# Kernel tuning notes

Measured on AMD Instinct MI355X. Metric: run time of the kernel, lower is better.

## Reference

```python
import jax, jax.numpy as jnp
import numpy as np

B, L, V, D = 8, 128, 32000, 64
R1, R2, UP = 2 * D, 5 * D, 10 * D  # first_reduce, second_reduce, up_scale defaults


def pos_enc(seq_len, d, n=10000.0):
    # matches getPositionEncoding: P[k,2i]=sin(k/n^(2i/d)), P[k,2i+1]=cos(k/n^(2i/d))
    k = jnp.arange(seq_len, dtype=jnp.float32)[:, None]
    i = jnp.arange(d // 2, dtype=jnp.float32)[None, :]
    ang = k / (n ** (2.0 * i / d))
    return jnp.stack([jnp.sin(ang), jnp.cos(ang)], axis=-1).reshape(seq_len, d)


def setup_inputs() -> dict:
    key = jax.random.key(0)
    ks = jax.random.split(key, 20)

    def lin(k, out_f, in_f):
        bound = 1.0 / np.sqrt(in_f)
        k1, k2 = jax.random.split(k)
        W = jax.random.uniform(k1, (out_f, in_f), jnp.float32, -bound, bound)
        b = jax.random.uniform(k2, (out_f,), jnp.float32, -bound, bound)
        return W, b

    inp = {"x": jax.random.uniform(ks[0], (B, L, V), jnp.float32)}
    inp["W_emb"], inp["b_emb"] = lin(ks[1], D, V)
    inp["W_pos1"], inp["b_pos1"] = lin(ks[2], D, 2 * D)
    inp["W_red"], inp["b_red"] = lin(ks[3], R1, L * D)
    inp["W_pos2"], inp["b_pos2"] = lin(ks[4], R1, 2 * R1)
    inp["W_red2"], inp["b_red2"] = lin(ks[5], R2, L * R1)
    inp["W_pos3"], inp["b_pos3"] = lin(ks[6], R2, 2 * R2)
    inp["W_up1"], inp["b_up1"] = lin(ks[7], UP, R2)
    inp["W_up2"], inp["b_up2"] = lin(ks[8], V, UP)
    inp["W_fin"], inp["b_fin"] = lin(ks[9], 1, L)
    return inp


def reference(x, W_emb, b_emb, W_pos1, b_pos1, W_red, b_red, W_pos2, b_pos2,
              W_red2, b_red2, W_pos3, b_pos3, W_up1, b_up1, W_up2, b_up2,
              W_fin, b_fin):
    relu = jax.nn.relu
    P1 = pos_enc(L, 2 * D)   # [L, 2D]
    P2 = pos_enc(L, 2 * R1)  # [L, 2*R1]
    P3 = pos_enc(L, 2 * R2)  # [L, 2*R2]

    h = relu(x @ W_emb.T + b_emb)                       # [B, L, D]
    h = h + relu(P1 @ W_pos1.T + b_pos1)[None]          # learned sin pos emb

    # einsum('bij,bkm->bikj'): out[b,i,k,j] = h[b,i,j] * sum_m h[b,k,m]
    s = h.sum(-1)                                       # [B, L]
    h = (h[:, :, None, :] * s[:, None, :, None]).reshape(B, L, L * D)
    h = relu(h @ W_red.T + b_red)                       # [B, L, R1]
    h = h + relu(P2 @ W_pos2.T + b_pos2)[None]

    s = h.sum(-1)                                       # [B, L]
    h = (h[:, :, None, :] * s[:, None, :, None]).reshape(B, L, L * R1)
    h = relu(h @ W_red2.T + b_red2)                     # [B, L, R2]
    h = h + relu(P3 @ W_pos3.T + b_pos3)[None]

    h = relu(h @ W_up1.T + b_up1)                       # [B, L, UP]
    h = relu(h @ W_up2.T + b_up2)                       # [B, L, V]
    # transpose(1,2) then Linear(L->1), relu, squeeze
    out = relu(jnp.einsum('blv,l->bv', h, W_fin[0]) + b_fin[0])  # [B, V]
    return out
```

## Files before the change

kernel.cpp:

```cpp
#include <hip/hip_runtime.h>
#include <hip/hip_bf16.h>
#include <math.h>

#define B_  8
#define L_  128
#define V_  32000
#define D_  64
#define R1_ 128
#define R2_ 320
#define UP_ 640
#define SPLITS_ 50

typedef short bf16x8 __attribute__((ext_vector_type(8)));
typedef float f32x4 __attribute__((ext_vector_type(4)));

#define GLDS16(gp, lp)                                                         \
    __builtin_amdgcn_global_load_lds(                                          \
        (const __attribute__((address_space(1))) void*)(gp),                   \
        (__attribute__((address_space(3))) void*)(lp), 16, 0, 0)

static __device__ inline unsigned short f2bf(float x) {
    __hip_bfloat16 h = __float2bfloat16(x);
    return *reinterpret_cast<unsigned short*>(&h);
}

static __device__ inline void split1(float v, unsigned short& h, unsigned short& l) {
    unsigned short hb = f2bf(v);
    float hf = __uint_as_float(((unsigned int)hb) << 16);
    h = hb;
    l = f2bf(v - hf);
}
static __device__ inline void split4(float4 v, ushort4& h, ushort4& l) {
    split1(v.x, h.x, l.x);
    split1(v.y, h.y, l.y);
    split1(v.z, h.z, l.z);
    split1(v.w, h.w, l.w);
}

__global__ __launch_bounds__(256) void pe_kernel(const float* __restrict__ W,
                                                 const float* __restrict__ bias,
                                                 float* __restrict__ out,
                                                 int outF, int dEnc) {
    __shared__ float P[640];
    int l = blockIdx.x;
    int t = threadIdx.x;
    for (int m = t; m < dEnc; m += 256) {
        int i = m >> 1;
        float ang = (float)l * powf(10000.0f, -2.0f * (float)i / (float)dEnc);
        P[m] = (m & 1) ? cosf(ang) : sinf(ang);
    }
    __syncthreads();
    for (int o = t; o < outF; o += 256) {
        float acc = bias[o];
        const float* w = W + (size_t)o * dEnc;
        for (int m = 0; m < dEnc; ++m) acc = fmaf(P[m], w[m], acc);
        out[l * outF + o] = fmaxf(acc, 0.f);
    }
}

__global__ __launch_bounds__(256) void embA_mfma(const float* __restrict__ x,
                                                 const float* __restrict__ Wemb,
                                                 float* __restrict__ partA) {
    __shared__ short lds[16384];
    const int XH = 0, XL = 4096, WH = 8192, WL = 12288;

    int t = threadIdx.x;
    int lane = t & 63, w = t >> 6;
    int ln = lane & 15, lg = lane >> 4;
    int sr = t >> 2, sc = t & 3;
    int rb = blockIdx.x, ks = blockIdx.y;
    int row0 = rb * 64;
    int mrow = w * 16 + ln;

    f32x4 acc[4];
#pragma unroll
    for (int nt = 0; nt < 4; ++nt) acc[nt] = (f32x4){0.f, 0.f, 0.f, 0.f};

    for (int ch = 0; ch < 640 / 64; ++ch) {
        int k0 = ks * 640 + ch * 64;
        const float* xrow = x + (size_t)(row0 + sr) * 32000 + k0;
        const float* wrow = Wemb + (size_t)sr * 32000 + k0;
        __syncthreads();
#pragma unroll
        for (int i = 0; i < 4; ++i) {
            int k = sc * 4 + 16 * i;
            int idx = ((k >> 3) * 64 + sr) * 8 + (k & 7);
            float4 v = *(const float4*)(xrow + k);
            ushort4 h, l;
            split4(v, h, l);
            *(ushort4*)&lds[XH + idx] = h;
            *(ushort4*)&lds[XL + idx] = l;
            float4 wv = *(const float4*)(wrow + k);
            split4(wv, h, l);
            *(ushort4*)&lds[WH + idx] = h;
            *(ushort4*)&lds[WL + idx] = l;
        }
        __syncthreads();
#pragma unroll
        for (int kstep = 0; kstep < 2; ++kstep) {
            int ga = kstep * 4 + lg;
            bf16x8 ah = *(const bf16x8*)&lds[XH + (ga * 64 + mrow) * 8];
            bf16x8 al = *(const bf16x8*)&lds[XL + (ga * 64 + mrow) * 8];
#pragma unroll
            for (int nt = 0; nt < 4; ++nt) {
                int nrow = nt * 16 + ln;
                bf16x8 bh = *(const bf16x8*)&lds[WH + (ga * 64 + nrow) * 8];
                bf16x8 bl = *(const bf16x8*)&lds[WL + (ga * 64 + nrow) * 8];
                acc[nt] = __builtin_amdgcn_mfma_f32_16x16x32_bf16(ah, bh, acc[nt], 0, 0, 0);
                acc[nt] = __builtin_amdgcn_mfma_f32_16x16x32_bf16(ah, bl, acc[nt], 0, 0, 0);
                acc[nt] = __builtin_amdgcn_mfma_f32_16x16x32_bf16(al, bh, acc[nt], 0, 0, 0);
            }
        }
    }
#pragma unroll
    for (int nt = 0; nt < 4; ++nt)
#pragma unroll
        for (int r = 0; r < 4; ++r)
            partA[((size_t)ks * 1024 + row0 + w * 16 + lg * 4 + r) * 64 + nt * 16 + ln] =
                acc[nt][r];
}

__global__ __launch_bounds__(64) void reduceA_kernel(const float* __restrict__ partA,
                                                     const float* __restrict__ bemb,
                                                     const float* __restrict__ pe1,
                                                     float* __restrict__ h1,
                                                     float* __restrict__ s1) {
    int row = blockIdx.x;
    int d = threadIdx.x;
    int l = row & 127;
    float v = bemb[d];
    for (int s = 0; s < SPLITS_; ++s) v += partA[((size_t)s * 1024 + row) * 64 + d];
    v = fmaxf(v, 0.f) + pe1[l * 64 + d];
    h1[row * 64 + d] = v;
    float sum = v;
    for (int off = 32; off > 0; off >>= 1) sum += __shfl_down(sum, off);
    if (d == 0) s1[row] = sum;
}

__global__ __launch_bounds__(64) void wr1_kernel(const float* __restrict__ Wred,
                                                 const float* __restrict__ s1,
                                                 float* __restrict__ Wr1) {
    __shared__ float ss[8 * 128];
    int r = blockIdx.x;
    int j = threadIdx.x;
    for (int idx = j; idx < 1024; idx += 64) ss[idx] = s1[idx];
    __syncthreads();
    float acc[8];
#pragma unroll
    for (int b = 0; b < 8; ++b) acc[b] = 0.f;
    const float* w = Wred + (size_t)r * 8192 + j;
    for (int k = 0; k < 128; ++k) {
        float wv = w[k * 64];
#pragma unroll
        for (int b = 0; b < 8; ++b) acc[b] = fmaf(ss[b * 128 + k], wv, acc[b]);
    }
#pragma unroll
    for (int b = 0; b < 8; ++b) Wr1[((size_t)b * 128 + r) * 64 + j] = acc[b];
}

__global__ __launch_bounds__(128) void h2_kernel(const float* __restrict__ h1,
                                                 const float* __restrict__ Wr1,
                                                 const float* __restrict__ bred,
                                                 const float* __restrict__ pe2,
                                                 float* __restrict__ h2,
                                                 float* __restrict__ s2) {
    __shared__ float hrow[64];
    __shared__ float red[2];
    int row = blockIdx.x;
    int b = row >> 7, i = row & 127;
    int r = threadIdx.x;
    if (r < 64) hrow[r] = h1[row * 64 + r];
    __syncthreads();
    float acc = bred[r];
    const float4* w = (const float4*)(Wr1 + ((size_t)b * 128 + r) * 64);
#pragma unroll
    for (int j4 = 0; j4 < 16; ++j4) {
        float4 wv = w[j4];
        float4 hv = *(const float4*)&hrow[j4 * 4];
        acc = fmaf(hv.x, wv.x, acc);
        acc = fmaf(hv.y, wv.y, acc);
        acc = fmaf(hv.z, wv.z, acc);
        acc = fmaf(hv.w, wv.w, acc);
    }
    float val = fmaxf(acc, 0.f) + pe2[i * 128 + r];
    h2[row * 128 + r] = val;
    float sum = val;
    for (int off = 32; off > 0; off >>= 1) sum += __shfl_down(sum, off);
    if ((r & 63) == 0) red[r >> 6] = sum;
    __syncthreads();
    if (r == 0) s2[row] = red[0] + red[1];
}

__global__ __launch_bounds__(128) void wr2_kernel(const float* __restrict__ Wred2,
                                                  const float* __restrict__ s2,
                                                  float* __restrict__ Wr2) {
    __shared__ float ss[8 * 128];
    int r = blockIdx.x;
    int j = threadIdx.x;
    for (int idx = j; idx < 1024; idx += 128) ss[idx] = s2[idx];
    __syncthreads();
    float acc[8];
#pragma unroll
    for (int b = 0; b < 8; ++b) acc[b] = 0.f;
    const float* w = Wred2 + (size_t)r * 16384 + j;
    for (int k = 0; k < 128; ++k) {
        float wv = w[k * 128];
#pragma unroll
        for (int b = 0; b < 8; ++b) acc[b] = fmaf(ss[b * 128 + k], wv, acc[b]);
    }
#pragma unroll
    for (int b = 0; b < 8; ++b) Wr2[((size_t)b * 320 + r) * 128 + j] = acc[b];
}

__global__ __launch_bounds__(320) void h3_kernel(const float* __restrict__ h2,
                                                 const float* __restrict__ Wr2,
                                                 const float* __restrict__ bred2,
                                                 const float* __restrict__ pe3,
                                                 float* __restrict__ h3) {
    __shared__ float hrow[128];
    int row = blockIdx.x;
    int b = row >> 7, i = row & 127;
    int r = threadIdx.x;
    if (r < 128) hrow[r] = h2[row * 128 + r];
    __syncthreads();
    float acc = bred2[r];
    const float4* w = (const float4*)(Wr2 + ((size_t)b * 320 + r) * 128);
#pragma unroll
    for (int j4 = 0; j4 < 32; ++j4) {
        float4 wv = w[j4];
        float4 hv = *(const float4*)&hrow[j4 * 4];
        acc = fmaf(hv.x, wv.x, acc);
        acc = fmaf(hv.y, wv.y, acc);
        acc = fmaf(hv.z, wv.z, acc);
        acc = fmaf(hv.w, wv.w, acc);
    }
    h3[(size_t)row * 320 + r] = fmaxf(acc, 0.f) + pe3[i * 320 + r];
}

__global__ __launch_bounds__(320) void h4_kernel(const float* __restrict__ h3,
                                                 const float* __restrict__ Wup1,
                                                 const float* __restrict__ bup1,
                                                 unsigned short* __restrict__ h4b) {
    __shared__ float hs[8 * 320];
    int rowbase = blockIdx.x * 8;
    int t = threadIdx.x;
    for (int idx = t; idx < 8 * 320; idx += 320) hs[idx] = h3[(size_t)rowbase * 320 + idx];
    __syncthreads();
    for (int uu = 0; uu < 2; ++uu) {
        int u = t + uu * 320;
        float bias = bup1[u];
        float acc[8];
#pragma unroll
        for (int q = 0; q < 8; ++q) acc[q] = bias;
        const float4* w = (const float4*)(Wup1 + (size_t)u * 320);
        for (int j4 = 0; j4 < 80; ++j4) {
            float4 wv = w[j4];
#pragma unroll
            for (int q = 0; q < 8; ++q) {
                float4 hv = *(const float4*)&hs[q * 320 + j4 * 4];
                acc[q] = fmaf(hv.x, wv.x, acc[q]);
                acc[q] = fmaf(hv.y, wv.y, acc[q]);
                acc[q] = fmaf(hv.z, wv.z, acc[q]);
                acc[q] = fmaf(hv.w, wv.w, acc[q]);
            }
        }
#pragma unroll
        for (int q = 0; q < 8; ++q)
            h4b[((size_t)rowbase + q) * 640 + u] = f2bf(fmaxf(acc[q], 0.f));
    }
}

__global__ __launch_bounds__(256) void conv_bf16(const float* __restrict__ src,
                                                 unsigned short* __restrict__ dst,
                                                 int n4) {
    int stride = gridDim.x * 256;
    for (int i = blockIdx.x * 256 + threadIdx.x; i < n4; i += stride) {
        float4 v = ((const float4*)src)[i];
        ushort4 o;
        o.x = f2bf(v.x); o.y = f2bf(v.y); o.z = f2bf(v.z); o.w = f2bf(v.w);
        ((ushort4*)dst)[i] = o;
    }
}

__global__ __launch_bounds__(256) void final_mfma_kernel(
    const unsigned short* __restrict__ h4b,
    const unsigned short* __restrict__ Wup2b,
    const float* __restrict__ bup2,
    const float* __restrict__ Wfin,
    const float* __restrict__ bfin,
    float* __restrict__ out) {
    __shared__ short tile[16384];
    __shared__ float redbuf[256];

    int t = threadIdx.x;
    int lane = t & 63;
    int w = t >> 6;
    int wv = w >> 1, wl = w & 1;
    int ln = lane & 15, lg = lane >> 4;
    int b = blockIdx.y;
    int v0 = blockIdx.x * 128;

    const char* Ag = (const char*)Wup2b;
    const char* Bg = (const char*)h4b;
    bool isA = (w < 2);
    int seg = (isA ? w : (w - 2)) * 8192;

    f32x4 acc[4][4];
#pragma unroll
    for (int mt = 0; mt < 4; ++mt)
#pragma unroll
        for (int nt = 0; nt < 4; ++nt) acc[mt][nt] = (f32x4){0.f, 0.f, 0.f, 0.f};

    for (int ch = 0; ch < 10; ++ch) {
        int k0 = ch * 64;
        __syncthreads();
#pragma unroll
        for (int s = 0; s < 8; ++s) {
            int F = seg + s * 1024 + lane * 16;
            int r = F >> 7;
            int g = ((F >> 4) & 7) ^ (r & 7);
            size_t rowG = isA ? (size_t)(v0 + r) : (size_t)(b * 128 + r);
            const char* gp = (isA ? Ag : Bg) + (rowG * 640 + (size_t)(k0 + g * 8)) * 2;
            char* lp = (char*)tile + (isA ? 0 : 16384) + seg + s * 1024;
            GLDS16(gp, lp);
        }
        __syncthreads();
#pragma unroll
        for (int ks = 0; ks < 2; ++ks) {
            bf16x8 aF[4], bF[4];
#pragma unroll
            for (int mt = 0; mt < 4; ++mt) {
                int rA = wv * 64 + mt * 16 + ln;
                int g = ks * 4 + lg;
                int off = rA * 128 + ((g ^ (rA & 7)) * 16);
                aF[mt] = *(const bf16x8*)((const char*)tile + off);
            }
#pragma unroll
            for (int nt = 0; nt < 4; ++nt) {
                int rB = wl * 64 + nt * 16 + ln;
                int g = ks * 4 + lg;
                int off = 16384 + rB * 128 + ((g ^ (rB & 7)) * 16);
                bF[nt] = *(const bf16x8*)((const char*)tile + off);
            }
#pragma unroll
            for (int mt = 0; mt < 4; ++mt)
#pragma unroll
                for (int nt = 0; nt < 4; ++nt)
                    acc[mt][nt] = __builtin_amdgcn_mfma_f32_16x16x32_bf16(
                        aF[mt], bF[nt], acc[mt][nt], 0, 0, 0);
        }
    }

    float bfin0 = bfin[0];
#pragma unroll
    for (int mt = 0; mt < 4; ++mt) {
        float bu[4];
#pragma unroll
        for (int r = 0; r < 4; ++r)
            bu[r] = bup2[v0 + wv * 64 + mt * 16 + lg * 4 + r];
        float part[4] = {0.f, 0.f, 0.f, 0.f};
#pragma unroll
        for (int nt = 0; nt < 4; ++nt) {
            float wf = Wfin[wl * 64 + nt * 16 + ln];
#pragma unroll
            for (int r = 0; r < 4; ++r)
                part[r] += wf * fmaxf(acc[mt][nt][r] + bu[r], 0.f);
        }
#pragma unroll
        for (int off = 8; off >= 1; off >>= 1)
#pragma unroll
            for (int r = 0; r < 4; ++r) part[r] += __shfl_xor(part[r], off, 64);
        if (ln == 0) {
#pragma unroll
            for (int r = 0; r < 4; ++r)
                redbuf[wl * 128 + wv * 64 + mt * 16 + lg * 4 + r] = part[r];
        }
    }
    __syncthreads();
    if (t < 128) {
        float vsum = redbuf[t] + redbuf[128 + t] + bfin0;
        out[(size_t)b * 32000 + v0 + t] = fmaxf(vsum, 0.f);
    }
}

extern "C" void kernel_launch(void* const* d_in, const int* in_sizes, int n_in,
                              void* d_out, int out_size, void* d_ws, size_t ws_size,
                              hipStream_t stream) {
    const float* x      = (const float*)d_in[0];
    const float* W_emb  = (const float*)d_in[1];
    const float* b_emb  = (const float*)d_in[2];
    const float* W_pos1 = (const float*)d_in[3];
    const float* b_pos1 = (const float*)d_in[4];
    const float* W_red  = (const float*)d_in[5];
    const float* b_red  = (const float*)d_in[6];
    const float* W_pos2 = (const float*)d_in[7];
    const float* b_pos2 = (const float*)d_in[8];
    const float* W_red2 = (const float*)d_in[9];
    const float* b_red2 = (const float*)d_in[10];
    const float* W_pos3 = (const float*)d_in[11];
    const float* b_pos3 = (const float*)d_in[12];
    const float* W_up1  = (const float*)d_in[13];
    const float* b_up1  = (const float*)d_in[14];
    const float* W_up2  = (const float*)d_in[15];
    const float* b_up2  = (const float*)d_in[16];
    const float* W_fin  = (const float*)d_in[17];
    const float* b_fin  = (const float*)d_in[18];
    float* out = (float*)d_out;

    float* ws  = (float*)d_ws;
    float* pe1 = ws;
    float* pe2 = pe1 + 8192;
    float* pe3 = pe2 + 16384;
    float* h1  = pe3 + 40960;
    float* s1  = h1 + 65536;
    float* Wr1 = s1 + 1024;
    float* h2  = Wr1 + 65536;
    float* s2  = h2 + 131072;
    float* Wr2 = s2 + 1024;
    float* h3  = Wr2 + 327680;
    unsigned short* h4b   = (unsigned short*)(h3 + 327680);
    unsigned short* Wup2b = (unsigned short*)((float*)h4b + 327680);
    float* partA = (float*)Wup2b;

    pe_kernel<<<dim3(128), 256, 0, stream>>>(W_pos1, b_pos1, pe1, 64, 128);
    pe_kernel<<<dim3(128), 256, 0, stream>>>(W_pos2, b_pos2, pe2, 128, 256);
    pe_kernel<<<dim3(128), 256, 0, stream>>>(W_pos3, b_pos3, pe3, 320, 640);
    embA_mfma<<<dim3(16, SPLITS_), 256, 0, stream>>>(x, W_emb, partA);
    reduceA_kernel<<<dim3(1024), 64, 0, stream>>>(partA, b_emb, pe1, h1, s1);
    conv_bf16<<<dim3(4096), 256, 0, stream>>>(W_up2, Wup2b, (V_ * UP_) / 4);
    wr1_kernel<<<dim3(128), 64, 0, stream>>>(W_red, s1, Wr1);
    h2_kernel<<<dim3(1024), 128, 0, stream>>>(h1, Wr1, b_red, pe2, h2, s2);
    wr2_kernel<<<dim3(320), 128, 0, stream>>>(W_red2, s2, Wr2);
    h3_kernel<<<dim3(1024), 320, 0, stream>>>(h2, Wr2, b_red2, pe3, h3);
    h4_kernel<<<dim3(128), 320, 0, stream>>>(h3, W_up1, b_up1, h4b);
    final_mfma_kernel<<<dim3(250, 8), 256, 0, stream>>>(h4b, Wup2b, b_up2, W_fin,
                                                        b_fin, out);
}
```

Before: 534.3 us.

## Pre-split W_emb to bf16, double-buffer embedding GEMM, transpose weights for coalescing

Pre-converts W_emb into hi/lo bf16 arrays in a separate kernel. The embedding GEMM then streams them into LDS with global_load_lds double buffering, while x is loaded into registers and split per lane. Split-K goes from 50 to 100 slices. W_pos and W_up1 are transposed so the pe and h4 kernels read coalesced columns, and h4 is regridded. This adds several extra preprocessing kernels and workspace each call, and doubles the partial-sum traffic in reduceA.

```diff
diff --git a/kernel.cpp b/kernel.cpp
--- a/kernel.cpp
+++ b/kernel.cpp
@@ -9,7 +9,7 @@
 #define R1_ 128
 #define R2_ 320
 #define UP_ 640
-#define SPLITS_ 50
+#define SPLITS_ 100
 
 typedef short bf16x8 __attribute__((ext_vector_type(8)));
 typedef float f32x4 __attribute__((ext_vector_type(4)));
@@ -30,87 +30,136 @@
     h = hb;
     l = f2bf(v - hf);
 }
-static __device__ inline void split4(float4 v, ushort4& h, ushort4& l) {
-    split1(v.x, h.x, l.x);
-    split1(v.y, h.y, l.y);
-    split1(v.z, h.z, l.z);
-    split1(v.w, h.w, l.w);
-}
-
-__global__ __launch_bounds__(256) void pe_kernel(const float* __restrict__ W,
+
+__global__ __launch_bounds__(256) void transpose_f32(const float* __restrict__ src,
+                                                     float* __restrict__ dst,
+                                                     int R, int C) {
+    int idx = blockIdx.x * 256 + threadIdx.x;
+    if (idx < R * C) {
+        int c = idx / R, r = idx - c * R;
+        dst[idx] = src[(size_t)r * C + c];
+    }
+}
+
+__global__ __launch_bounds__(256) void convW_emb(const float* __restrict__ Wemb,
+                                                 unsigned short* __restrict__ Whb,
+                                                 unsigned short* __restrict__ Wlb) {
+    int u = blockIdx.x * 256 + threadIdx.x;
+    int kb = u >> 6, row = u & 63;
+    const float* s = Wemb + (size_t)row * 32000 + kb * 8;
+    unsigned short h8[8], l8[8];
+#pragma unroll
+    for (int j = 0; j < 8; ++j) split1(s[j], h8[j], l8[j]);
+    *(ushort4*)&Whb[(size_t)u * 8]     = *(ushort4*)&h8[0];
+    *(ushort4*)&Whb[(size_t)u * 8 + 4] = *(ushort4*)&h8[4];
+    *(ushort4*)&Wlb[(size_t)u * 8]     = *(ushort4*)&l8[0];
+    *(ushort4*)&Wlb[(size_t)u * 8 + 4] = *(ushort4*)&l8[4];
+}
+
+__global__ __launch_bounds__(320) void pe_kernel(const float* __restrict__ WT,
                                                  const float* __restrict__ bias,
                                                  float* __restrict__ out,
                                                  int outF, int dEnc) {
     __shared__ float P[640];
     int l = blockIdx.x;
     int t = threadIdx.x;
-    for (int m = t; m < dEnc; m += 256) {
+    for (int m = t; m < dEnc; m += outF) {
         int i = m >> 1;
         float ang = (float)l * powf(10000.0f, -2.0f * (float)i / (float)dEnc);
         P[m] = (m & 1) ? cosf(ang) : sinf(ang);
     }
     __syncthreads();
-    for (int o = t; o < outF; o += 256) {
-        float acc = bias[o];
-        const float* w = W + (size_t)o * dEnc;
-        for (int m = 0; m < dEnc; ++m) acc = fmaf(P[m], w[m], acc);
-        out[l * outF + o] = fmaxf(acc, 0.f);
-    }
+    float acc = bias[t];
+#pragma unroll 4
+    for (int m = 0; m < dEnc; ++m) acc = fmaf(P[m], WT[(size_t)m * outF + t], acc);
+    out[l * outF + t] = fmaxf(acc, 0.f);
 }
 
 __global__ __launch_bounds__(256) void embA_mfma(const float* __restrict__ x,
-                                                 const float* __restrict__ Wemb,
+                                                 const unsigned short* __restrict__ Whb,
+                                                 const unsigned short* __restrict__ Wlb,
                                                  float* __restrict__ partA) {
     __shared__ short lds[16384];
-    const int XH = 0, XL = 4096, WH = 8192, WL = 12288;
-
     int t = threadIdx.x;
     int lane = t & 63, w = t >> 6;
     int ln = lane & 15, lg = lane >> 4;
-    int sr = t >> 2, sc = t & 3;
     int rb = blockIdx.x, ks = blockIdx.y;
     int row0 = rb * 64;
-    int mrow = w * 16 + ln;
+    const float* xrow = x + (size_t)(row0 + w * 16 + ln) * 32000;
 
     f32x4 acc[4];
 #pragma unroll
     for (int nt = 0; nt < 4; ++nt) acc[nt] = (f32x4){0.f, 0.f, 0.f, 0.f};
 
-    for (int ch = 0; ch < 640 / 64; ++ch) {
-        int k0 = ks * 640 + ch * 64;
-        const float* xrow = x + (size_t)(row0 + sr) * 32000 + k0;
-        const float* wrow = Wemb + (size_t)sr * 32000 + k0;
+    float4 xc[4], xn[4];
+
+    {
+        int kb0 = (ks * 320) >> 3;
+#pragma unroll
+        for (int s = 0; s < 4; ++s) {
+            int ubase = s * 256 + w * 64;
+            const unsigned short* arr = (s < 2) ? Whb : Wlb;
+            int uu = (s < 2) ? ubase : (ubase - 512);
+            const char* gp = (const char*)arr + ((size_t)kb0 * 64 + uu + lane) * 16;
+            char* lp = (char*)lds + ((s < 2) ? 0 : 8192) + uu * 16;
+            GLDS16(gp, lp);
+        }
+        const float* bp = xrow + ks * 320 + lg * 8;
+        xc[0] = ((const float4*)bp)[0];
+        xc[1] = ((const float4*)bp)[1];
+        xc[2] = ((const float4*)(bp + 32))[0];
+        xc[3] = ((const float4*)(bp + 32))[1];
+    }
+
+#pragma unroll
+    for (int ch = 0; ch < 5; ++ch) {
         __syncthreads();
-#pragma unroll
-        for (int i = 0; i < 4; ++i) {
-            int k = sc * 4 + 16 * i;
-            int idx = ((k >> 3) * 64 + sr) * 8 + (k & 7);
-            float4 v = *(const float4*)(xrow + k);
-            ushort4 h, l;
-            split4(v, h, l);
-            *(ushort4*)&lds[XH + idx] = h;
-            *(ushort4*)&lds[XL + idx] = l;
-            float4 wv = *(const float4*)(wrow + k);
-            split4(wv, h, l);
-            *(ushort4*)&lds[WH + idx] = h;
-            *(ushort4*)&lds[WL + idx] = l;
-        }
-        __syncthreads();
+        if (ch < 4) {
+            int kb0 = (ks * 320 + (ch + 1) * 64) >> 3;
+            int p = (ch + 1) & 1;
+#pragma unroll
+            for (int s = 0; s < 4; ++s) {
+                int ubase = s * 256 + w * 64;
+                const unsigned short* arr = (s < 2) ? Whb : Wlb;
+                int uu = (s < 2) ? ubase : (ubase - 512);
+                const char* gp = (const char*)arr + ((size_t)kb0 * 64 + uu + lane) * 16;
+                char* lp = (char*)lds + p * 16384 + ((s < 2) ? 0 : 8192) + uu * 16;
+                GLDS16(gp, lp);
+            }
+            const float* bp = xrow + ks * 320 + (ch + 1) * 64 + lg * 8;
+            xn[0] = ((const float4*)bp)[0];
+            xn[1] = ((const float4*)bp)[1];
+            xn[2] = ((const float4*)(bp + 32))[0];
+            xn[3] = ((const float4*)(bp + 32))[1];
+        }
+        bf16x8 ah[2], al[2];
 #pragma unroll
         for (int kstep = 0; kstep < 2; ++kstep) {
-            int ga = kstep * 4 + lg;
-            bf16x8 ah = *(const bf16x8*)&lds[XH + (ga * 64 + mrow) * 8];
-            bf16x8 al = *(const bf16x8*)&lds[XL + (ga * 64 + mrow) * 8];
+            float f[8] = {xc[2 * kstep].x, xc[2 * kstep].y, xc[2 * kstep].z, xc[2 * kstep].w,
+                          xc[2 * kstep + 1].x, xc[2 * kstep + 1].y, xc[2 * kstep + 1].z,
+                          xc[2 * kstep + 1].w};
+            unsigned short h8[8], l8[8];
+#pragma unroll
+            for (int j = 0; j < 8; ++j) split1(f[j], h8[j], l8[j]);
+            ah[kstep] = *(bf16x8*)h8;
+            al[kstep] = *(bf16x8*)l8;
+        }
+        const char* buf = (const char*)lds + (ch & 1) * 16384;
+#pragma unroll
+        for (int kstep = 0; kstep < 2; ++kstep) {
+            int g = kstep * 4 + lg;
 #pragma unroll
             for (int nt = 0; nt < 4; ++nt) {
                 int nrow = nt * 16 + ln;
-                bf16x8 bh = *(const bf16x8*)&lds[WH + (ga * 64 + nrow) * 8];
-                bf16x8 bl = *(const bf16x8*)&lds[WL + (ga * 64 + nrow) * 8];
-                acc[nt] = __builtin_amdgcn_mfma_f32_16x16x32_bf16(ah, bh, acc[nt], 0, 0, 0);
-                acc[nt] = __builtin_amdgcn_mfma_f32_16x16x32_bf16(ah, bl, acc[nt], 0, 0, 0);
-                acc[nt] = __builtin_amdgcn_mfma_f32_16x16x32_bf16(al, bh, acc[nt], 0, 0, 0);
+                bf16x8 bh = *(const bf16x8*)(buf + (g * 64 + nrow) * 16);
+                bf16x8 bl = *(const bf16x8*)(buf + 8192 + (g * 64 + nrow) * 16);
+                acc[nt] = __builtin_amdgcn_mfma_f32_16x16x32_bf16(ah[kstep], bh, acc[nt], 0, 0, 0);
+                acc[nt] = __builtin_amdgcn_mfma_f32_16x16x32_bf16(ah[kstep], bl, acc[nt], 0, 0, 0);
+                acc[nt] = __builtin_amdgcn_mfma_f32_16x16x32_bf16(al[kstep], bh, acc[nt], 0, 0, 0);
             }
         }
+#pragma unroll
+        for (int i = 0; i < 4; ++i) xc[i] = xn[i];
     }
 #pragma unroll
     for (int nt = 0; nt < 4; ++nt)
@@ -129,6 +178,7 @@
     int d = threadIdx.x;
     int l = row & 127;
     float v = bemb[d];
+#pragma unroll 4
     for (int s = 0; s < SPLITS_; ++s) v += partA[((size_t)s * 1024 + row) * 64 + d];
     v = fmaxf(v, 0.f) + pe1[l * 64 + d];
     h1[row * 64 + d] = v;
@@ -238,36 +288,33 @@
 }
 
 __global__ __launch_bounds__(320) void h4_kernel(const float* __restrict__ h3,
-                                                 const float* __restrict__ Wup1,
+                                                 const float* __restrict__ Wup1T,
                                                  const float* __restrict__ bup1,
                                                  unsigned short* __restrict__ h4b) {
-    __shared__ float hs[8 * 320];
-    int rowbase = blockIdx.x * 8;
+    __shared__ float hsT[320 * 4];
     int t = threadIdx.x;
-    for (int idx = t; idx < 8 * 320; idx += 320) hs[idx] = h3[(size_t)rowbase * 320 + idx];
-    __syncthreads();
-    for (int uu = 0; uu < 2; ++uu) {
-        int u = t + uu * 320;
-        float bias = bup1[u];
-        float acc[8];
-#pragma unroll
-        for (int q = 0; q < 8; ++q) acc[q] = bias;
-        const float4* w = (const float4*)(Wup1 + (size_t)u * 320);
-        for (int j4 = 0; j4 < 80; ++j4) {
-            float4 wv = w[j4];
-#pragma unroll
-            for (int q = 0; q < 8; ++q) {
-                float4 hv = *(const float4*)&hs[q * 320 + j4 * 4];
-                acc[q] = fmaf(hv.x, wv.x, acc[q]);
-                acc[q] = fmaf(hv.y, wv.y, acc[q]);
-                acc[q] = fmaf(hv.z, wv.z, acc[q]);
-                acc[q] = fmaf(hv.w, wv.w, acc[q]);
-            }
-        }
-#pragma unroll
-        for (int q = 0; q < 8; ++q)
-            h4b[((size_t)rowbase + q) * 640 + u] = f2bf(fmaxf(acc[q], 0.f));
-    }
+    int row0 = blockIdx.x * 4;
+    int u = blockIdx.y * 320 + t;
+    for (int idx = t; idx < 1280; idx += 320) {
+        int q = idx / 320, j = idx - q * 320;
+        hsT[j * 4 + q] = h3[(size_t)(row0 + q) * 320 + j];
+    }
+    __syncthreads();
+    float acc[4] = {0.f, 0.f, 0.f, 0.f};
+    const float* wt = Wup1T + u;
+#pragma unroll 4
+    for (int j = 0; j < 320; ++j) {
+        float wv = wt[(size_t)j * 640];
+        float4 hv = *(const float4*)&hsT[j * 4];
+        acc[0] = fmaf(hv.x, wv, acc[0]);
+        acc[1] = fmaf(hv.y, wv, acc[1]);
+        acc[2] = fmaf(hv.z, wv, acc[2]);
+        acc[3] = fmaf(hv.w, wv, acc[3]);
+    }
+    float bias = bup1[u];
+#pragma unroll
+    for (int q = 0; q < 4; ++q)
+        h4b[(size_t)(row0 + q) * 640 + u] = f2bf(fmaxf(acc[q] + bias, 0.f));
 }
 
 __global__ __launch_bounds__(256) void conv_bf16(const float* __restrict__ src,
@@ -420,19 +467,33 @@
     float* h3  = Wr2 + 327680;
     unsigned short* h4b   = (unsigned short*)(h3 + 327680);
     unsigned short* Wup2b = (unsigned short*)((float*)h4b + 327680);
+    float* after = (float*)Wup2b + 10240000;
+    float* WposT1 = after;
+    float* WposT2 = WposT1 + 8192;
+    float* WposT3 = WposT2 + 32768;
+    float* Wup1T  = WposT3 + 204800;
+    unsigned short* Whb = (unsigned short*)(Wup1T + 204800);
+    unsigned short* Wlb = Whb + 2048000;
     float* partA = (float*)Wup2b;
 
-    pe_kernel<<<dim3(128), 256, 0, stream>>>(W_pos1, b_pos1, pe1, 64, 128);
-    pe_kernel<<<dim3(128), 256, 0, stream>>>(W_pos2, b_pos2, pe2, 128, 256);
-    pe_kernel<<<dim3(128), 256, 0, stream>>>(W_pos3, b_pos3, pe3, 320, 640);
-    embA_mfma<<<dim3(16, SPLITS_), 256, 0, stream>>>(x, W_emb, partA);
+    convW_emb<<<dim3(1000), 256, 0, stream>>>(W_emb, Whb, Wlb);
+    transpose_f32<<<dim3(32), 256, 0, stream>>>(W_pos1, WposT1, 64, 128);
+    transpose_f32<<<dim3(128), 256, 0, stream>>>(W_pos2, WposT2, 128, 256);
+    transpose_f32<<<dim3(800), 256, 0, stream>>>(W_pos3, WposT3, 320, 640);
+    transpose_f32<<<dim3(800), 256, 0, stream>>>(W_up1, Wup1T, 640, 320);
+
+    pe_kernel<<<dim3(128), 64, 0, stream>>>(WposT1, b_pos1, pe1, 64, 128);
+    pe_kernel<<<dim3(128), 128, 0, stream>>>(WposT2, b_pos2, pe2, 128, 256);
+    pe_kernel<<<dim3(128), 320, 0, stream>>>(WposT3, b_pos3, pe3, 320, 640);
+
+    embA_mfma<<<dim3(16, SPLITS_), 256, 0, stream>>>(x, Whb, Wlb, partA);
     reduceA_kernel<<<dim3(1024), 64, 0, stream>>>(partA, b_emb, pe1, h1, s1);
     conv_bf16<<<dim3(4096), 256, 0, stream>>>(W_up2, Wup2b, (V_ * UP_) / 4);
     wr1_kernel<<<dim3(128), 64, 0, stream>>>(W_red, s1, Wr1);
     h2_kernel<<<dim3(1024), 128, 0, stream>>>(h1, Wr1, b_red, pe2, h2, s2);
     wr2_kernel<<<dim3(320), 128, 0, stream>>>(W_red2, s2, Wr2);
     h3_kernel<<<dim3(1024), 320, 0, stream>>>(h2, Wr2, b_red2, pe3, h3);
-    h4_kernel<<<dim3(128), 320, 0, stream>>>(h3, W_up1, b_up1, h4b);
+    h4_kernel<<<dim3(256, 2), 320, 0, stream>>>(h3, Wup1T, b_up1, h4b);
     final_mfma_kernel<<<dim3(250, 8), 256, 0, stream>>>(h4b, Wup2b, b_up2, W_fin,
                                                         b_fin, out);
 }
```

Measured after the change: 559.5 us. +4.7%, slower.
